# Kernel optimization log

Measured on AMD Instinct MI355X. Metric: run time of the kernel, lower is better.

## Reference

```python
import jax, jax.numpy as jnp
import numpy as np

BS = 128          # block size for fp8 block-scaled quantization
FP8_MAX = 448.0   # max normal value of float8_e4m3fn


def _weight_quant(w):
    """Quantize weight [O, I] with per-(128x128)-block scales, DeepSeek-V3 style.
    Returns (w_q stored as fp32 holding fp8-representable values, scale [O/BS, I/BS])."""
    O, I = w.shape
    wb = w.reshape(O // BS, BS, I // BS, BS)
    amax = jnp.max(jnp.abs(wb), axis=(1, 3))
    scale = jnp.where(amax == 0, 1.0, amax / FP8_MAX)
    q = (wb / scale[:, None, :, None]).astype(jnp.float8_e4m3fn).astype(jnp.float32)
    return q.reshape(O, I), scale


def _act_qdq(x):
    """act_quant + dequant: per-128-block (last dim) fp8 quantization of activations."""
    T, D = x.shape
    xb = x.reshape(T, D // BS, BS)
    amax = jnp.max(jnp.abs(xb), axis=-1, keepdims=True)
    scale = jnp.where(amax == 0, 1.0, amax / FP8_MAX)
    q = (xb / scale).astype(jnp.float8_e4m3fn).astype(jnp.float32)
    return (q * scale).reshape(T, D)


def _dequant_w(wq, ws):
    O, I = wq.shape
    return (wq.reshape(O // BS, BS, I // BS, BS) * ws[:, None, :, None]).reshape(O, I)


def _linear_fp8(x, wq, ws):
    # fp8_gemm with per-block scales == dequantized GEMM in fp32 accumulate
    return _act_qdq(x) @ _dequant_w(wq, ws).T


def setup_inputs() -> dict:
    T, DIM, INTER = 2048, 4096, 11008
    key = jax.random.key(0)
    kx, k1, k2, k3 = jax.random.split(key, 4)
    x = jax.random.normal(kx, (T, DIM), dtype=jnp.float32)
    w1 = jax.random.normal(k1, (INTER, DIM), dtype=jnp.float32) * 0.02
    w2 = jax.random.normal(k2, (DIM, INTER), dtype=jnp.float32) * 0.02
    w3 = jax.random.normal(k3, (INTER, DIM), dtype=jnp.float32) * 0.02
    w1_q, w1_s = _weight_quant(w1)
    w2_q, w2_s = _weight_quant(w2)
    w3_q, w3_s = _weight_quant(w3)
    return {"x": x, "w1_q": w1_q, "w1_s": w1_s, "w2_q": w2_q, "w2_s": w2_s,
            "w3_q": w3_q, "w3_s": w3_s}


def reference(x, w1_q, w1_s, w2_q, w2_s, w3_q, w3_s):
    # SwiGLU: w2( silu(w1(x)) * w3(x) ), each linear is fp8 block-scaled GEMM
    h = jax.nn.silu(_linear_fp8(x, w1_q, w1_s)) * _linear_fp8(x, w3_q, w3_s)
    return _linear_fp8(h, w2_q, w2_s)
```

## Files before the change

kernel.cpp:

```cpp
#include <hip/hip_runtime.h>
#include <hip/hip_fp8.h>
#include <hip/hip_fp16.h>

#define T_DIM 2048
#define D_DIM 4096
#define I_DIM 11008

typedef int v8i __attribute__((ext_vector_type(8)));
typedef int v4i __attribute__((ext_vector_type(4)));
typedef float v4f __attribute__((ext_vector_type(4)));

__device__ inline unsigned char to_fp8(float f) {
  return (unsigned char)__hip_cvt_float_to_fp8(f, __HIP_SATFINITE, __HIP_E4M3);
}

__device__ inline void async_copy16(const void* g, void* l) {
  __builtin_amdgcn_global_load_lds((const __attribute__((address_space(1))) void*)g,
                                   (__attribute__((address_space(3))) void*)l, 16, 0, 0);
}

__global__ void quant_x_kernel(const float* __restrict__ X, unsigned char* __restrict__ Q,
                               float* __restrict__ St, const int T, const int D) {
  const int wave = (blockIdx.x << 2) + (threadIdx.x >> 6);
  const int lane = threadIdx.x & 63;
  const int nb = D >> 7;
  const int t = wave / nb;
  const int kb = wave - t * nb;
  const size_t base = (size_t)t * D + ((size_t)kb << 7);
  const float2 v = ((const float2*)(X + base))[lane];
  float a = fmaxf(fabsf(v.x), fabsf(v.y));
#pragma unroll
  for (int off = 32; off > 0; off >>= 1) a = fmaxf(a, __shfl_xor(a, off));
  const float scale = (a == 0.f) ? 1.f : (a / 448.f);
  unsigned short pk = (unsigned short)to_fp8(v.x / scale) |
                      ((unsigned short)to_fp8(v.y / scale) << 8);
  ((unsigned short*)(Q + base))[lane] = pk;
  if (lane == 0) St[(size_t)kb * T + t] = scale;
}

__global__ void silu_mul_quant_kernel(const __half* __restrict__ H1, const __half* __restrict__ H3,
                                      unsigned char* __restrict__ Q, float* __restrict__ St,
                                      const int T, const int D) {
  const int wave = (blockIdx.x << 2) + (threadIdx.x >> 6);
  const int lane = threadIdx.x & 63;
  const int nb = D >> 7;
  const int t = wave / nb;
  const int kb = wave - t * nb;
  const size_t base = (size_t)t * D + ((size_t)kb << 7);
  const float2 v1 = __half22float2(((const __half2*)(H1 + base))[lane]);
  const float2 v3 = __half22float2(((const __half2*)(H3 + base))[lane]);
  const float hx = (v1.x / (1.f + expf(-v1.x))) * v3.x;
  const float hy = (v1.y / (1.f + expf(-v1.y))) * v3.y;
  float a = fmaxf(fabsf(hx), fabsf(hy));
#pragma unroll
  for (int off = 32; off > 0; off >>= 1) a = fmaxf(a, __shfl_xor(a, off));
  const float scale = (a == 0.f) ? 1.f : (a / 448.f);
  unsigned short pk = (unsigned short)to_fp8(hx / scale) |
                      ((unsigned short)to_fp8(hy / scale) << 8);
  ((unsigned short*)(Q + base))[lane] = pk;
  if (lane == 0) St[(size_t)kb * T + t] = scale;
}

__global__ void convert3_fp8_kernel(const float4* __restrict__ W1, const float4* __restrict__ W3,
                                    const float4* __restrict__ W2, unsigned int* __restrict__ Q1,
                                    unsigned int* __restrict__ Q3, unsigned int* __restrict__ Q2,
                                    const int n4) {
  const int i = blockIdx.x * 256 + threadIdx.x;
  if (i >= n4) return;
  const int sel = blockIdx.y;
  const float4* src = (sel == 0) ? W1 : (sel == 1) ? W3 : W2;
  unsigned int* dst = (sel == 0) ? Q1 : (sel == 1) ? Q3 : Q2;
  const float4 f = src[i];
  dst[i] = (unsigned int)to_fp8(f.x) | ((unsigned int)to_fp8(f.y) << 8) |
           ((unsigned int)to_fp8(f.z) << 16) | ((unsigned int)to_fp8(f.w) << 24);
}

template <int MI, typename CT>
__global__ __launch_bounds__(512, 2) void gemm256_fp8_bs(
    const unsigned char* __restrict__ A, const float* __restrict__ sAt,
    const unsigned char* __restrict__ Ba, const float* __restrict__ sBa, CT* __restrict__ Ca,
    const unsigned char* __restrict__ Bb, const float* __restrict__ sBb, CT* __restrict__ Cb,
    const int NY, const int M, const int N, const int K) {
  constexpr int BM = MI * 32;
  constexpr int AT = MI / 2;
  __shared__ __align__(16) unsigned char As[2][BM * 128];
  __shared__ __align__(16) unsigned char Bs[2][256 * 128];
  __shared__ __align__(16) float sAs[2][BM];
  __shared__ float sbl[192];

  const int tid = threadIdx.x;
  const int lane = tid & 63;
  const int w = tid >> 6;
  const int wm = w >> 2;
  const int wn = w & 3;
  const int wmrow = wm * (MI << 4);
  const int wnrow = wn << 6;
  const int row16 = lane & 15;
  const int quad = lane >> 4;
  const int nkb = K >> 7;

  int by = (int)blockIdx.y;
  const int sel = by >= NY;
  if (sel) by -= NY;
  const unsigned char* B = sel ? Bb : Ba;
  const float* sB = sel ? sBb : sBa;
  CT* C = sel ? Cb : Ca;
  const int m0 = (int)blockIdx.x * BM;
  const int n0 = by << 8;

  {
    const float* p0 = sB + (size_t)(n0 >> 7) * nkb;
    if (tid < 2 * nkb) sbl[tid] = p0[tid];
  }

  const int srow = tid >> 3;
  const int gcol = (((tid & 7) ^ (srow & 7)) << 4);
  const unsigned char* gA = A + (size_t)(m0 + srow) * K + gcol;
  const unsigned char* gB = B + (size_t)(n0 + srow) * K + gcol;
  const float* gSa = sAt + m0 + w * (BM / 8) + (lane << 2);

  const int off0 = (((quad << 1) ^ (row16 & 7)) << 4);
  const int off1 = off0 ^ 16;

  v4f zero = {0.f, 0.f, 0.f, 0.f};
  v4f acc[MI][4];
#pragma unroll
  for (int i = 0; i < MI; ++i)
#pragma unroll
    for (int j = 0; j < 4; ++j) acc[i][j] = zero;

#define STAGE(c, kb_)                                                           \
  {                                                                             \
    const size_t koff_ = (size_t)(kb_) << 7;                                    \
    _Pragma("unroll") for (int t_ = 0; t_ < AT; ++t_)                           \
        async_copy16(gA + koff_ + ((size_t)(t_ << 6)) * K,                      \
                     &As[c][(t_ << 13) + (w << 10)]);                           \
    _Pragma("unroll") for (int t_ = 0; t_ < 4; ++t_)                            \
        async_copy16(gB + koff_ + ((size_t)(t_ << 6)) * K,                      \
                     &Bs[c][(t_ << 13) + (w << 10)]);                           \
    if (lane < BM / 32) async_copy16(gSa + (size_t)(kb_) * M, &sAs[c][w * (BM / 8)]); \
  }

#define LDA(dst, AP, mi)                                                        \
  {                                                                             \
    const unsigned char* p_ = (AP) + ((wmrow + ((mi) << 4) + row16) << 7);      \
    const v4i lo_ = *(const v4i*)(p_ + off0);                                   \
    const v4i hi_ = *(const v4i*)(p_ + off1);                                   \
    dst = __builtin_shufflevector(lo_, hi_, 0, 1, 2, 3, 4, 5, 6, 7);            \
  }

#define LDB(dst, BP, nj)                                                        \
  {                                                                             \
    const unsigned char* p_ = (BP) + ((wnrow + ((nj) << 4) + row16) << 7);      \
    const v4i lo_ = *(const v4i*)(p_ + off0);                                   \
    const v4i hi_ = *(const v4i*)(p_ + off1);                                   \
    dst = __builtin_shufflevector(lo_, hi_, 0, 1, 2, 3, 4, 5, 6, 7);            \
  }

#define LDCS(H)                                                                 \
  {                                                                             \
    const float4 s0_ = *(const float4*)(Sc + wmrow + ((H) << 6) + (quad << 2)); \
    const float4 s1_ = *(const float4*)(Sc + wmrow + ((H) << 6) + 16 + (quad << 2)); \
    const float4 s2_ = *(const float4*)(Sc + wmrow + ((H) << 6) + 32 + (quad << 2)); \
    const float4 s3_ = *(const float4*)(Sc + wmrow + ((H) << 6) + 48 + (quad << 2)); \
    cs0 = (v4f){s0_.x * sb, s0_.y * sb, s0_.z * sb, s0_.w * sb};                \
    cs1 = (v4f){s1_.x * sb, s1_.y * sb, s1_.z * sb, s1_.w * sb};                \
    cs2 = (v4f){s2_.x * sb, s2_.y * sb, s2_.z * sb, s2_.w * sb};                \
    cs3 = (v4f){s3_.x * sb, s3_.y * sb, s3_.z * sb, s3_.w * sb};                \
  }

#define MFMA1(af, bf)                                                           \
  __builtin_amdgcn_mfma_scale_f32_16x16x128_f8f6f4((af), (bf), zero, 0, 0, 0,   \
                                                   0x7f7f7f7f, 0, 0x7f7f7f7f)

#define MFMA_BATCH(H, bL, bR, jL, jR)                                           \
  {                                                                             \
    v4f p0_ = MFMA1(a0, bL);                                                    \
    v4f p1_ = MFMA1(a0, bR);                                                    \
    v4f p2_ = MFMA1(a1, bL);                                                    \
    v4f p3_ = MFMA1(a1, bR);                                                    \
    v4f p4_ = MFMA1(a2, bL);                                                    \
    v4f p5_ = MFMA1(a2, bR);                                                    \
    v4f p6_ = MFMA1(a3, bL);                                                    \
    v4f p7_ = MFMA1(a3, bR);                                                    \
    acc[(H)*4 + 0][jL] += cs0 * p0_;                                            \
    acc[(H)*4 + 0][jR] += cs0 * p1_;                                            \
    acc[(H)*4 + 1][jL] += cs1 * p2_;                                            \
    acc[(H)*4 + 1][jR] += cs1 * p3_;                                            \
    acc[(H)*4 + 2][jL] += cs2 * p4_;                                            \
    acc[(H)*4 + 2][jR] += cs2 * p5_;                                            \
    acc[(H)*4 + 3][jL] += cs3 * p6_;                                            \
    acc[(H)*4 + 3][jR] += cs3 * p7_;                                            \
  }

  __syncthreads();

  STAGE(0, 0);

  const int sbi = (wn >> 1) * nkb;

  for (int kb = 0; kb < nkb; ++kb) {
    const int cur = kb & 1;
    if (kb + 1 < nkb) {
      STAGE(cur ^ 1, kb + 1);
      if constexpr (MI == 8) {
        asm volatile("s_waitcnt vmcnt(9)" ::: "memory");
      } else {
        asm volatile("s_waitcnt vmcnt(7)" ::: "memory");
      }
    } else {
      asm volatile("s_waitcnt vmcnt(0)" ::: "memory");
    }
    __builtin_amdgcn_s_barrier();
    __builtin_amdgcn_sched_barrier(0);

    const unsigned char* Ac = As[cur];
    const unsigned char* Bc = Bs[cur];
    const float* Sc = sAs[cur];
    const float sb = sbl[sbi + kb];
    v8i a0, a1, a2, a3, b0, b1, b2, b3;
    v4f cs0, cs1, cs2, cs3;

    LDB(b0, Bc, 0); LDB(b1, Bc, 1); LDB(b2, Bc, 2); LDB(b3, Bc, 3);

    LDA(a0, Ac, 0); LDA(a1, Ac, 1); LDA(a2, Ac, 2); LDA(a3, Ac, 3);
    LDCS(0);
    MFMA_BATCH(0, b0, b1, 0, 1);
    MFMA_BATCH(0, b2, b3, 2, 3);

    if constexpr (MI == 8) {
      LDA(a0, Ac, 4); LDA(a1, Ac, 5); LDA(a2, Ac, 6); LDA(a3, Ac, 7);
      LDCS(1);
      MFMA_BATCH(1, b0, b1, 0, 1);
      MFMA_BATCH(1, b2, b3, 2, 3);
    }

    asm volatile("s_waitcnt lgkmcnt(0)" ::: "memory");
    __builtin_amdgcn_s_barrier();
    __builtin_amdgcn_sched_barrier(0);
  }

#undef STAGE
#undef LDA
#undef LDB
#undef LDCS
#undef MFMA1
#undef MFMA_BATCH

#pragma unroll
  for (int mi = 0; mi < MI; ++mi) {
    const size_t rb = (size_t)(m0 + wmrow + (mi << 4) + (quad << 2));
#pragma unroll
    for (int r = 0; r < 4; ++r) {
      CT* crow = C + (rb + r) * N + n0 + wnrow + row16;
#pragma unroll
      for (int nj = 0; nj < 4; ++nj) crow[nj << 4] = (CT)acc[mi][nj][r];
    }
  }
}

extern "C" void kernel_launch(void* const* d_in, const int* in_sizes, int n_in,
                              void* d_out, int out_size, void* d_ws, size_t ws_size,
                              hipStream_t stream) {
  const float* x   = (const float*)d_in[0];
  const float* w1q = (const float*)d_in[1];
  const float* w1s = (const float*)d_in[2];
  const float* w2q = (const float*)d_in[3];
  const float* w2s = (const float*)d_in[4];
  const float* w3q = (const float*)d_in[5];
  const float* w3s = (const float*)d_in[6];

  unsigned char* ws = (unsigned char*)d_ws;
  const size_t SZ_QX = (size_t)T_DIM * D_DIM;
  const size_t SZ_W  = (size_t)I_DIM * D_DIM;
  const size_t SZ_QH = (size_t)T_DIM * I_DIM;
  const size_t SZ_SX = (size_t)(D_DIM / 128) * T_DIM * 4;
  const size_t SZ_SH = (size_t)(I_DIM / 128) * T_DIM * 4;
  const size_t SZ_H  = (size_t)T_DIM * I_DIM * 2;

  unsigned char* qx   = ws;             ws += SZ_QX;
  unsigned char* w1q8 = ws;             ws += SZ_W;
  unsigned char* w3q8 = ws;             ws += SZ_W;
  unsigned char* w2q8 = ws;             ws += SZ_W;
  unsigned char* qh   = ws;             ws += SZ_QH;
  float* sxt = (float*)ws;              ws += SZ_SX;
  float* sht = (float*)ws;              ws += SZ_SH;
  __half* h1 = (__half*)ws;             ws += SZ_H;
  __half* h3 = (__half*)ws;             ws += SZ_H;

  quant_x_kernel<<<(T_DIM * (D_DIM / 128)) / 4, 256, 0, stream>>>(x, qx, sxt, T_DIM, D_DIM);

  const int n4w = (int)(SZ_W / 4);
  dim3 gc(n4w / 256, 3);
  convert3_fp8_kernel<<<gc, 256, 0, stream>>>((const float4*)w1q, (const float4*)w3q,
                                              (const float4*)w2q, (unsigned int*)w1q8,
                                              (unsigned int*)w3q8, (unsigned int*)w2q8, n4w);

  dim3 g13(T_DIM / 256, 2 * (I_DIM / 256));
  gemm256_fp8_bs<8, __half><<<g13, 512, 0, stream>>>(qx, sxt,
                                                     w1q8, w1s, h1,
                                                     w3q8, w3s, h3,
                                                     I_DIM / 256, T_DIM, I_DIM, D_DIM);

  silu_mul_quant_kernel<<<(T_DIM * (I_DIM / 128)) / 4, 256, 0, stream>>>(h1, h3, qh, sht, T_DIM, I_DIM);

  dim3 g2(T_DIM / 128, D_DIM / 256);
  gemm256_fp8_bs<4, float><<<g2, 512, 0, stream>>>(qh, sht,
                                                   w2q8, w2s, (float*)d_out,
                                                   w2q8, w2s, (float*)d_out,
                                                   D_DIM / 256, T_DIM, D_DIM, I_DIM);

  (void)in_sizes; (void)n_in; (void)out_size; (void)ws_size;
}
```

Measured before the change: 1.142 ms.

## Load B operand directly from global into registers, bypassing LDS

The B tile is no longer staged through shared memory. Each wave loads its own B fragments straight from global memory into registers, double-buffered across even and odd k-blocks with a loop unrolled by two, while A still goes through async LDS copies. This halves LDS traffic and footprint, and launch bounds drop to one block per SM to make room for the extra registers. The cost is redundant global reads of B across the wave rows and lower occupancy, and the loop assumes an even number of k-blocks.

```diff
diff --git a/kernel.cpp b/kernel.cpp
--- a/kernel.cpp
+++ b/kernel.cpp
@@ -76,7 +76,7 @@
 }
 
 template <int MI, typename CT>
-__global__ __launch_bounds__(512, 2) void gemm256_fp8_bs(
+__global__ __launch_bounds__(512, 1) void gemm256_fp8_bs(
     const unsigned char* __restrict__ A, const float* __restrict__ sAt,
     const unsigned char* __restrict__ Ba, const float* __restrict__ sBa, CT* __restrict__ Ca,
     const unsigned char* __restrict__ Bb, const float* __restrict__ sBb, CT* __restrict__ Cb,
@@ -84,7 +84,6 @@
   constexpr int BM = MI * 32;
   constexpr int AT = MI / 2;
   __shared__ __align__(16) unsigned char As[2][BM * 128];
-  __shared__ __align__(16) unsigned char Bs[2][256 * 128];
   __shared__ __align__(16) float sAs[2][BM];
   __shared__ float sbl[192];
 
@@ -116,8 +115,9 @@
   const int srow = tid >> 3;
   const int gcol = (((tid & 7) ^ (srow & 7)) << 4);
   const unsigned char* gA = A + (size_t)(m0 + srow) * K + gcol;
-  const unsigned char* gB = B + (size_t)(n0 + srow) * K + gcol;
   const float* gSa = sAt + m0 + w * (BM / 8) + (lane << 2);
+
+  const unsigned char* gBr = B + (size_t)(n0 + wnrow + row16) * K + (quad << 5);
 
   const int off0 = (((quad << 1) ^ (row16 & 7)) << 4);
   const int off1 = off0 ^ 16;
@@ -129,29 +129,34 @@
 #pragma unroll
     for (int j = 0; j < 4; ++j) acc[i][j] = zero;
 
-#define STAGE(c, kb_)                                                           \
+  v4i bE0, bE1, bE2, bE3, bE4, bE5, bE6, bE7;
+  v4i bO0, bO1, bO2, bO3, bO4, bO5, bO6, bO7;
+
+#define STAGE_A(c, kb_)                                                         \
   {                                                                             \
     const size_t koff_ = (size_t)(kb_) << 7;                                    \
     _Pragma("unroll") for (int t_ = 0; t_ < AT; ++t_)                           \
         async_copy16(gA + koff_ + ((size_t)(t_ << 6)) * K,                      \
                      &As[c][(t_ << 13) + (w << 10)]);                           \
-    _Pragma("unroll") for (int t_ = 0; t_ < 4; ++t_)                            \
-        async_copy16(gB + koff_ + ((size_t)(t_ << 6)) * K,                      \
-                     &Bs[c][(t_ << 13) + (w << 10)]);                           \
     if (lane < BM / 32) async_copy16(gSa + (size_t)(kb_) * M, &sAs[c][w * (BM / 8)]); \
   }
 
+#define BLOAD(S, kb_)                                                           \
+  {                                                                             \
+    const unsigned char* pb_ = gBr + ((size_t)(kb_) << 7);                      \
+    S##0 = *(const v4i*)(pb_);                                                  \
+    S##1 = *(const v4i*)(pb_ + 16);                                             \
+    S##2 = *(const v4i*)(pb_ + (size_t)16 * K);                                 \
+    S##3 = *(const v4i*)(pb_ + (size_t)16 * K + 16);                            \
+    S##4 = *(const v4i*)(pb_ + (size_t)32 * K);                                 \
+    S##5 = *(const v4i*)(pb_ + (size_t)32 * K + 16);                            \
+    S##6 = *(const v4i*)(pb_ + (size_t)48 * K);                                 \
+    S##7 = *(const v4i*)(pb_ + (size_t)48 * K + 16);                            \
+  }
+
 #define LDA(dst, AP, mi)                                                        \
   {                                                                             \
     const unsigned char* p_ = (AP) + ((wmrow + ((mi) << 4) + row16) << 7);      \
-    const v4i lo_ = *(const v4i*)(p_ + off0);                                   \
-    const v4i hi_ = *(const v4i*)(p_ + off1);                                   \
-    dst = __builtin_shufflevector(lo_, hi_, 0, 1, 2, 3, 4, 5, 6, 7);            \
-  }
-
-#define LDB(dst, BP, nj)                                                        \
-  {                                                                             \
-    const unsigned char* p_ = (BP) + ((wnrow + ((nj) << 4) + row16) << 7);      \
     const v4i lo_ = *(const v4i*)(p_ + off0);                                   \
     const v4i hi_ = *(const v4i*)(p_ + off1);                                   \
     dst = __builtin_shufflevector(lo_, hi_, 0, 1, 2, 3, 4, 5, 6, 7);            \
@@ -193,59 +198,81 @@
     acc[(H)*4 + 3][jR] += cs3 * p7_;                                            \
   }
 
+#define COMPUTE_TILE(c, kb_, S)                                                 \
+  {                                                                             \
+    const unsigned char* Ac = &As[c][0];                                        \
+    const float* Sc = &sAs[c][0];                                               \
+    const float sb = sbl[sbi + (kb_)];                                          \
+    v8i b0 = __builtin_shufflevector(S##0, S##1, 0, 1, 2, 3, 4, 5, 6, 7);       \
+    v8i b1 = __builtin_shufflevector(S##2, S##3, 0, 1, 2, 3, 4, 5, 6, 7);       \
+    v8i b2 = __builtin_shufflevector(S##4, S##5, 0, 1, 2, 3, 4, 5, 6, 7);       \
+    v8i b3 = __builtin_shufflevector(S##6, S##7, 0, 1, 2, 3, 4, 5, 6, 7);       \
+    v8i a0, a1, a2, a3;                                                         \
+    v4f cs0, cs1, cs2, cs3;                                                     \
+    LDA(a0, Ac, 0); LDA(a1, Ac, 1); LDA(a2, Ac, 2); LDA(a3, Ac, 3);             \
+    LDCS(0);                                                                    \
+    MFMA_BATCH(0, b0, b1, 0, 1);                                                \
+    MFMA_BATCH(0, b2, b3, 2, 3);                                                \
+    if constexpr (MI == 8) {                                                    \
+      LDA(a0, Ac, 4); LDA(a1, Ac, 5); LDA(a2, Ac, 6); LDA(a3, Ac, 7);           \
+      LDCS(1);                                                                  \
+      MFMA_BATCH(1, b0, b1, 0, 1);                                              \
+      MFMA_BATCH(1, b2, b3, 2, 3);                                              \
+    }                                                                           \
+  }
+
+#define WAIT_STEADY                                                             \
+  do {                                                                          \
+    if constexpr (MI == 8) {                                                    \
+      asm volatile("s_waitcnt vmcnt(13)" ::: "memory");                         \
+    } else {                                                                    \
+      asm volatile("s_waitcnt vmcnt(11)" ::: "memory");                         \
+    }                                                                           \
+  } while (0)
+
   __syncthreads();
 
-  STAGE(0, 0);
+  STAGE_A(0, 0);
+  BLOAD(bE, 0);
 
   const int sbi = (wn >> 1) * nkb;
 
-  for (int kb = 0; kb < nkb; ++kb) {
-    const int cur = kb & 1;
-    if (kb + 1 < nkb) {
-      STAGE(cur ^ 1, kb + 1);
-      if constexpr (MI == 8) {
-        asm volatile("s_waitcnt vmcnt(9)" ::: "memory");
-      } else {
-        asm volatile("s_waitcnt vmcnt(7)" ::: "memory");
-      }
+  for (int kb = 0; kb < nkb; kb += 2) {
+    STAGE_A(1, kb + 1);
+    BLOAD(bO, kb + 1);
+    __builtin_amdgcn_sched_barrier(0);
+    WAIT_STEADY;
+    __builtin_amdgcn_s_barrier();
+    __builtin_amdgcn_sched_barrier(0);
+    COMPUTE_TILE(0, kb, bE);
+    asm volatile("s_waitcnt lgkmcnt(0)" ::: "memory");
+    __builtin_amdgcn_s_barrier();
+    __builtin_amdgcn_sched_barrier(0);
+
+    if (kb + 2 < nkb) {
+      STAGE_A(0, kb + 2);
+      BLOAD(bE, kb + 2);
+      __builtin_amdgcn_sched_barrier(0);
+      WAIT_STEADY;
     } else {
       asm volatile("s_waitcnt vmcnt(0)" ::: "memory");
     }
     __builtin_amdgcn_s_barrier();
     __builtin_amdgcn_sched_barrier(0);
-
-    const unsigned char* Ac = As[cur];
-    const unsigned char* Bc = Bs[cur];
-    const float* Sc = sAs[cur];
-    const float sb = sbl[sbi + kb];
-    v8i a0, a1, a2, a3, b0, b1, b2, b3;
-    v4f cs0, cs1, cs2, cs3;
-
-    LDB(b0, Bc, 0); LDB(b1, Bc, 1); LDB(b2, Bc, 2); LDB(b3, Bc, 3);
-
-    LDA(a0, Ac, 0); LDA(a1, Ac, 1); LDA(a2, Ac, 2); LDA(a3, Ac, 3);
-    LDCS(0);
-    MFMA_BATCH(0, b0, b1, 0, 1);
-    MFMA_BATCH(0, b2, b3, 2, 3);
-
-    if constexpr (MI == 8) {
-      LDA(a0, Ac, 4); LDA(a1, Ac, 5); LDA(a2, Ac, 6); LDA(a3, Ac, 7);
-      LDCS(1);
-      MFMA_BATCH(1, b0, b1, 0, 1);
-      MFMA_BATCH(1, b2, b3, 2, 3);
-    }
-
+    COMPUTE_TILE(1, kb + 1, bO);
     asm volatile("s_waitcnt lgkmcnt(0)" ::: "memory");
     __builtin_amdgcn_s_barrier();
     __builtin_amdgcn_sched_barrier(0);
   }
 
-#undef STAGE
+#undef STAGE_A
+#undef BLOAD
 #undef LDA
-#undef LDB
 #undef LDCS
 #undef MFMA1
 #undef MFMA_BATCH
+#undef COMPUTE_TILE
+#undef WAIT_STEADY
 
 #pragma unroll
   for (int mi = 0; mi < MI; ++mi) {
```

After: 2.501 ms. +119.0%, slower.
